# Performance work log

Hardware: AMD Instinct MI355X
Metric: run time of the kernel (lower is better)

The kernel has to match this reference:

```python
import jax, jax.numpy as jnp
import numpy as np

HEAD_SIZE = 12
INNER_DIM = 64
BIG_NEG = 1e12


def _sinusoidal(seq_len, dim):
    # interleaved [sin, cos, sin, cos, ...] like SinusoidalPositionEmbedding('zero')
    pos = jnp.arange(seq_len, dtype=jnp.float32)
    inv = jnp.power(10000.0, -2.0 * jnp.arange(dim // 2, dtype=jnp.float32) / dim)
    ang = pos[:, None] * inv[None, :]                       # (L, dim/2)
    return jnp.stack([jnp.sin(ang), jnp.cos(ang)], axis=-1).reshape(seq_len, dim)


def _rope_rotate(x, cos_pos, sin_pos):
    # x: (B, L, H, D); rotate-half per interleaved RoPE
    x2 = jnp.stack([-x[..., 1::2], x[..., ::2]], axis=-1).reshape(x.shape)
    return x * cos_pos + x2 * sin_pos


def setup_inputs() -> dict:
    key = jax.random.key(0)
    k1, k2 = jax.random.split(key)
    B, L, HID = 16, 512, 768
    sequence_output = jax.random.normal(k1, (B, L, HID), dtype=jnp.float32)
    mask = jnp.ones((B, L), dtype=jnp.float32)
    W = jax.random.normal(k2, (HID, HEAD_SIZE * INNER_DIM * 2), dtype=jnp.float32) * 0.02
    b = jnp.zeros((HEAD_SIZE * INNER_DIM * 2,), dtype=jnp.float32)
    return {"sequence_output": sequence_output, "mask": mask, "W": W, "b": b}


def reference(sequence_output, mask, W, b):
    B, L, _ = sequence_output.shape
    H, D = HEAD_SIZE, INNER_DIM
    out = sequence_output @ W + b                           # (B, L, H*2D)
    out = out.reshape(B, L, H, 2 * D)
    qw, kw = out[..., :D], out[..., D:]                     # (B, L, H, D)
    pos = _sinusoidal(L, D)                                 # (L, D)
    cos_pos = jnp.repeat(pos[:, None, 1::2], 2, axis=-1)    # (L, 1, D)
    sin_pos = jnp.repeat(pos[:, None, ::2], 2, axis=-1)
    qw = _rope_rotate(qw, cos_pos, sin_pos)
    kw = _rope_rotate(kw, cos_pos, sin_pos)
    logits = jnp.einsum('bmhd,bnhd->bhmn', qw, kw)          # (B, H, L, L)
    pad = mask[:, None, None, :]                            # (B, 1, 1, L)
    logits = logits * pad - (1.0 - pad) * BIG_NEG
    tril = jnp.tril(jnp.ones((L, L), dtype=logits.dtype), -1)
    logits = logits - tril * BIG_NEG
    return logits / (D ** 0.5)
```

## Files before the change

### kernel.cpp

```cpp
#include <hip/hip_runtime.h>
#include <stdint.h>

typedef float f32x4 __attribute__((ext_vector_type(4)));
typedef unsigned long long u64;

#define HEADS 12
#define DDIM 64
#define LSEQ 512
#define HID 768
#define NOUT 1536
#define BIG_NEG 1000000000000.0f

__device__ __forceinline__ void gl_lds16(const void* g, void* l) {
    __builtin_amdgcn_global_load_lds(
        (const __attribute__((address_space(1))) void*)g,
        (__attribute__((address_space(3))) void*)l, 16, 0, 0);
}

__device__ __forceinline__ void ldsbar() {
    asm volatile("s_waitcnt lgkmcnt(0)" ::: "memory");
    __builtin_amdgcn_s_barrier();
}

__device__ __forceinline__ uint32_t pk4_fp8(float a, float b, float c, float d) {
    uint32_t v = __builtin_amdgcn_cvt_pk_fp8_f32(a, b, 0, false);
    v = __builtin_amdgcn_cvt_pk_fp8_f32(c, d, v, true);
    return v;
}

__global__ __launch_bounds__(256) void prep_k(
    const float* __restrict__ X, const float* __restrict__ W,
    uint8_t* __restrict__ Xq, uint8_t* __restrict__ Wtq,
    float* __restrict__ cosT, float* __restrict__ sinT) {

    int blk = blockIdx.x;
    if (blk < 3072) {
        size_t idx = ((size_t)blk * 256 + threadIdx.x) * 8;
        float4 f0 = *(const float4*)(X + idx);
        float4 f1 = *(const float4*)(X + idx + 4);
        uint2 p;
        p.x = pk4_fp8(f0.x, f0.y, f0.z, f0.w);
        p.y = pk4_fp8(f1.x, f1.y, f1.z, f1.w);
        *(uint2*)(Xq + idx) = p;
    } else if (blk < 4224) {
        __shared__ float Ls[32][33];
        int b2 = blk - 3072;
        int n0 = (b2 % 48) * 32, k0 = (b2 / 48) * 32;
        int tx = threadIdx.x & 31, ty = threadIdx.x >> 5;
#pragma unroll
        for (int rr = 0; rr < 4; ++rr) {
            int k = ty + rr * 8;
            Ls[k][tx] = W[(size_t)(k0 + k) * NOUT + n0 + tx];
        }
        __syncthreads();
        int n = threadIdx.x >> 3, c = threadIdx.x & 7;
        uint32_t w = pk4_fp8(Ls[4*c][n], Ls[4*c+1][n], Ls[4*c+2][n], Ls[4*c+3][n]);
        *(uint32_t*)(Wtq + (size_t)(n0 + n) * HID + k0 + c * 4) = w;
    } else {
        int idx = (blk - 4224) * 256 + threadIdx.x;
        int l = idx >> 6, d = idx & 63;
        int p = d >> 1;
        float inv = powf(10000.0f, (-2.0f * (float)p) / 64.0f);
        float ang = (float)l * inv;
        cosT[idx] = cosf(ang);
        sinT[idx] = sinf(ang);
    }
}

__global__ __launch_bounds__(256) void proj_rope_k(
    const uint8_t* __restrict__ Xq, const uint8_t* __restrict__ Wtq,
    const float* __restrict__ bias, const float* __restrict__ cosT,
    const float* __restrict__ sinT,
    uint8_t* __restrict__ qq, uint8_t* __restrict__ kq) {

    __shared__ __align__(16) uint8_t As[128 * 64];
    __shared__ __align__(16) uint8_t Bs[128 * 64];

    const int tid = threadIdx.x;
    const int m0 = blockIdx.x * 128, n0 = blockIdx.y * 128;
    const int lane = tid & 63, wid = tid >> 6;
    const int wm = wid >> 1, wn = wid & 1;
    const int lr = lane & 15, kg = lane >> 4;

    const int srow = tid >> 2, sc = tid & 3;

    f32x4 acc[4][4] = {};

    for (int k0 = 0; k0 < HID; k0 += 64) {
#pragma unroll
        for (int j = 0; j < 2; ++j) {
            int r = j * 64 + srow;
            int cs = sc ^ ((r >> 1) & 3);
            gl_lds16(Wtq + (size_t)(n0 + r) * HID + k0 + cs * 16,
                     Bs + j * 4096 + tid * 16);
            gl_lds16(Xq + (size_t)(m0 + r) * HID + k0 + cs * 16,
                     As + j * 4096 + tid * 16);
        }
        __syncthreads();
#pragma unroll
        for (int ks = 0; ks < 2; ++ks) {
            u64 af[4], xf[4];
#pragma unroll
            for (int ai = 0; ai < 4; ++ai) {
                int row = wn * 64 + ai * 16 + lr;
                int sl = (ks * 4 + kg) ^ (row & 6);
                af[ai] = *(const u64*)(Bs + row * 64 + sl * 8);
            }
#pragma unroll
            for (int bi = 0; bi < 4; ++bi) {
                int row = wm * 64 + bi * 16 + lr;
                int sl = (ks * 4 + kg) ^ (row & 6);
                xf[bi] = *(const u64*)(As + row * 64 + sl * 8);
            }
#pragma unroll
            for (int ai = 0; ai < 4; ++ai)
#pragma unroll
                for (int bi = 0; bi < 4; ++bi)
                    acc[ai][bi] = __builtin_amdgcn_mfma_f32_16x16x32_fp8_fp8(
                        (long long)af[ai], (long long)xf[bi], acc[ai][bi], 0, 0, 0);
        }
        __syncthreads();
    }

#pragma unroll
    for (int ai = 0; ai < 4; ++ai) {
        int nb = n0 + wn * 64 + ai * 16 + kg * 4;
        int h = nb >> 7, d2 = nb & 127;
        int d = d2 & 63;
        uint8_t* dst = (d2 >= 64) ? kq : qq;
        float4 b4 = *(const float4*)&bias[nb];
#pragma unroll
        for (int bi = 0; bi < 4; ++bi) {
            int m = m0 + wm * 64 + bi * 16 + lr;
            int bidx = m >> 9, lpos = m & 511;
            float4 c4 = *(const float4*)&cosT[lpos * 64 + d];
            float4 s4 = *(const float4*)&sinT[lpos * 64 + d];
            float v0 = acc[ai][bi][0] + b4.x;
            float v1 = acc[ai][bi][1] + b4.y;
            float v2 = acc[ai][bi][2] + b4.z;
            float v3 = acc[ai][bi][3] + b4.w;
            float o0 = v0 * c4.x - v1 * s4.x;
            float o1 = v1 * c4.y + v0 * s4.y;
            float o2 = v2 * c4.z - v3 * s4.z;
            float o3 = v3 * c4.w + v2 * s4.w;
            uint32_t pw = pk4_fp8(o0, o1, o2, o3);
            *(uint32_t*)(dst + (((size_t)bidx * HEADS + h) * LSEQ + lpos) * DDIM + d) = pw;
        }
    }
}

__global__ __launch_bounds__(256) void attn_k(
    const uint8_t* __restrict__ qq, const uint8_t* __restrict__ kq,
    const float* __restrict__ mask, float* __restrict__ out) {

    __shared__ __align__(16) uint8_t Qs[8192];
    __shared__ __align__(16) uint8_t Ks[8192];
    __shared__ __align__(16) float Es[32 * 132];
    __shared__ int wok[4];

    const int tid = threadIdx.x;
    const int bid = blockIdx.x;
    const int L = (bid & 7) * 96 + (bid >> 3);
    const int bh = L >> 2;
    const int mtile = L & 3;
    const int m0 = mtile * 128;
    const int lane = tid & 63, wid = tid >> 6;
    const int wm = wid >> 1, wn = wid & 1;
    const int lr = lane & 15, kg = lane >> 4;
    const int b = bh / HEADS;

    int myok = 1;
    for (int c0 = tid; c0 < m0; c0 += 256)
        myok &= (mask[b * LSEQ + c0] == 1.0f) ? 1 : 0;
    unsigned long long bal = __ballot(myok);
    if (lane == 0) wok[wid] = (bal == ~0ull) ? 1 : 0;
    ldsbar();
    const int nstart = (wok[0] & wok[1] & wok[2] & wok[3]) ? mtile : 0;

    const uint8_t* qbase = qq + ((size_t)bh * LSEQ + m0) * DDIM;
    const uint8_t* kbase = kq + (size_t)bh * LSEQ * DDIM;

    const int srow = tid >> 2, sc = tid & 3;
#pragma unroll
    for (int j = 0; j < 2; ++j) {
        int r = j * 64 + srow;
        int cs = sc ^ ((r >> 1) & 3);
        gl_lds16(qbase + (size_t)r * DDIM + cs * 16, Qs + j * 4096 + tid * 16);
        gl_lds16(kbase + (size_t)(nstart * 128 + r) * DDIM + cs * 16,
                 Ks + j * 4096 + tid * 16);
    }
    __syncthreads();

    const int colb = (tid & 31) * 4;
    const int rrow = tid >> 5;
    float* obase = out + (size_t)bh * LSEQ * LSEQ;

    for (int nt = nstart; nt < 4; ++nt) {
        f32x4 acc[4][4] = {};
#pragma unroll
        for (int ks = 0; ks < 2; ++ks) {
            u64 af[4], qf[4];
#pragma unroll
            for (int ai = 0; ai < 4; ++ai) {
                int row = wn * 64 + ai * 16 + lr;
                int sl = (ks * 4 + kg) ^ (row & 6);
                af[ai] = *(const u64*)(Ks + row * 64 + sl * 8);
            }
#pragma unroll
            for (int bi = 0; bi < 4; ++bi) {
                int row = wm * 64 + bi * 16 + lr;
                int sl = (ks * 4 + kg) ^ (row & 6);
                qf[bi] = *(const u64*)(Qs + row * 64 + sl * 8);
            }
#pragma unroll
            for (int ai = 0; ai < 4; ++ai)
#pragma unroll
                for (int bi = 0; bi < 4; ++bi)
                    acc[ai][bi] = __builtin_amdgcn_mfma_f32_16x16x32_fp8_fp8(
                        (long long)af[ai], (long long)qf[bi], acc[ai][bi], 0, 0, 0);
        }
        ldsbar();

        const int n0 = nt * 128;
        const float4 p4 = *(const float4*)&mask[b * LSEQ + n0 + colb];

        if (nt < 3) {
#pragma unroll
            for (int j = 0; j < 2; ++j) {
                int r = j * 64 + srow;
                int cs = sc ^ ((r >> 1) & 3);
                gl_lds16(kbase + (size_t)((nt + 1) * 128 + r) * DDIM + cs * 16,
                         Ks + j * 4096 + tid * 16);
            }
        }

#pragma unroll
        for (int p = 0; p < 4; ++p) {
            ldsbar();
            if (wm == (p >> 1)) {
                const int bi0 = (p & 1) * 2;
#pragma unroll
                for (int bb = 0; bb < 2; ++bb) {
                    int bi = bi0 + bb;
                    int row = bb * 16 + lr;
#pragma unroll
                    for (int ai = 0; ai < 4; ++ai) {
                        int n = wn * 64 + ai * 16 + kg * 4;
                        *(f32x4*)&Es[row * 132 + n] = acc[ai][bi];
                    }
                }
            }
            ldsbar();
#pragma unroll
            for (int j = 0; j < 4; ++j) {
                int rloc = rrow + j * 8;
                int m = m0 + p * 32 + rloc;
                f32x4 v = *(f32x4*)&Es[rloc * 132 + colb];
                int n = n0 + colb;
                f32x4 o;
                o[0] = (v[0] * p4.x - (1.0f - p4.x) * BIG_NEG
                        - ((m > n + 0) ? BIG_NEG : 0.0f)) * 0.125f;
                o[1] = (v[1] * p4.y - (1.0f - p4.y) * BIG_NEG
                        - ((m > n + 1) ? BIG_NEG : 0.0f)) * 0.125f;
                o[2] = (v[2] * p4.z - (1.0f - p4.z) * BIG_NEG
                        - ((m > n + 2) ? BIG_NEG : 0.0f)) * 0.125f;
                o[3] = (v[3] * p4.w - (1.0f - p4.w) * BIG_NEG
                        - ((m > n + 3) ? BIG_NEG : 0.0f)) * 0.125f;
                __builtin_nontemporal_store(o, (f32x4*)&obase[(size_t)m * LSEQ + n]);
            }
        }

        if (nt < 3) {
            asm volatile("s_waitcnt vmcnt(16) lgkmcnt(0)" ::: "memory");
            __builtin_amdgcn_s_barrier();
        }
    }

    const float CONSTV = (-BIG_NEG) * 0.125f;
    f32x4 cv = {CONSTV, CONSTV, CONSTV, CONSTV};
    for (int nt2 = 0; nt2 < nstart; ++nt2) {
        int n = nt2 * 128 + colb;
#pragma unroll
        for (int p = 0; p < 4; ++p)
#pragma unroll
            for (int j = 0; j < 4; ++j) {
                int m = m0 + p * 32 + rrow + j * 8;
                __builtin_nontemporal_store(cv, (f32x4*)&obase[(size_t)m * LSEQ + n]);
            }
    }
}

extern "C" void kernel_launch(void* const* d_in, const int* in_sizes, int n_in,
                              void* d_out, int out_size, void* d_ws, size_t ws_size,
                              hipStream_t stream) {
    const float* X    = (const float*)d_in[0];
    const float* mask = (const float*)d_in[1];
    const float* W    = (const float*)d_in[2];
    const float* bias = (const float*)d_in[3];
    float* out = (float*)d_out;

    char* ws = (char*)d_ws;
    float*   cosT = (float*)ws;
    float*   sinT = (float*)(ws + 131072);
    uint8_t* Wtq  = (uint8_t*)(ws + 262144);
    uint8_t* Xq   = (uint8_t*)(ws + 1441792);
    uint8_t* qq   = (uint8_t*)(ws + 7733248);
    uint8_t* kq   = (uint8_t*)(ws + 14024704);

    prep_k<<<4352, 256, 0, stream>>>(X, W, Xq, Wtq, cosT, sinT);
    proj_rope_k<<<dim3(64, 12), 256, 0, stream>>>(Xq, Wtq, bias, cosT, sinT, qq, kq);
    attn_k<<<768, 256, 0, stream>>>(qq, kq, mask, out);
}
```

Baseline: 83.54 us.

## Use 32x32 fp8 MFMA with Q in registers and direct scalar output stores

Rewrites the attention-logit kernel so each wave owns 32 query rows held in registers and runs 32x32x16 fp8 MFMAs against K tiles in LDS. The LDS staging buffer and its barrier-heavy transpose epilogue are dropped in favor of storing accumulators straight to global memory as scalar nontemporal stores. It also adds a fast path for an all-ones mask that skips the padding arithmetic. The cost removed is LDS round trips and barriers in the epilogue, at the price of 4-byte stores that coalesce only 32 floats per row instead of 16-byte vector stores.

```diff
diff --git a/kernel.cpp b/kernel.cpp
--- a/kernel.cpp
+++ b/kernel.cpp
@@ -2,6 +2,7 @@
 #include <stdint.h>
 
 typedef float f32x4 __attribute__((ext_vector_type(4)));
+typedef float f32x16 __attribute__((ext_vector_type(16)));
 typedef unsigned long long u64;
 
 #define HEADS 12
@@ -10,6 +11,7 @@
 #define HID 768
 #define NOUT 1536
 #define BIG_NEG 1000000000000.0f
+#define BIGS 125000000000.0f
 
 __device__ __forceinline__ void gl_lds16(const void* g, void* l) {
     __builtin_amdgcn_global_load_lds(
@@ -153,10 +155,9 @@
     const uint8_t* __restrict__ qq, const uint8_t* __restrict__ kq,
     const float* __restrict__ mask, float* __restrict__ out) {
 
-    __shared__ __align__(16) uint8_t Qs[8192];
     __shared__ __align__(16) uint8_t Ks[8192];
-    __shared__ __align__(16) float Es[32 * 132];
     __shared__ int wok[4];
+    __shared__ int wall[4];
 
     const int tid = threadIdx.x;
     const int bid = blockIdx.x;
@@ -165,19 +166,23 @@
     const int mtile = L & 3;
     const int m0 = mtile * 128;
     const int lane = tid & 63, wid = tid >> 6;
-    const int wm = wid >> 1, wn = wid & 1;
-    const int lr = lane & 15, kg = lane >> 4;
+    const int li = lane & 31, hi = lane >> 5;
     const int b = bh / HEADS;
 
-    int myok = 1;
-    for (int c0 = tid; c0 < m0; c0 += 256)
-        myok &= (mask[b * LSEQ + c0] == 1.0f) ? 1 : 0;
-    unsigned long long bal = __ballot(myok);
-    if (lane == 0) wok[wid] = (bal == ~0ull) ? 1 : 0;
+    int myok = 1, myall = 1;
+    for (int c0 = tid; c0 < LSEQ; c0 += 256) {
+        int one = (mask[b * LSEQ + c0] == 1.0f) ? 1 : 0;
+        myall &= one;
+        if (c0 < m0) myok &= one;
+    }
+    unsigned long long balok = __ballot(myok);
+    unsigned long long balall = __ballot(myall);
+    if (lane == 0) { wok[wid] = (balok == ~0ull); wall[wid] = (balall == ~0ull); }
     ldsbar();
     const int nstart = (wok[0] & wok[1] & wok[2] & wok[3]) ? mtile : 0;
-
-    const uint8_t* qbase = qq + ((size_t)bh * LSEQ + m0) * DDIM;
+    const int allones = wall[0] & wall[1] & wall[2] & wall[3];
+
+    const uint8_t* qbase = qq + ((size_t)bh * LSEQ + m0 + wid * 32) * DDIM;
     const uint8_t* kbase = kq + (size_t)bh * LSEQ * DDIM;
 
     const int srow = tid >> 2, sc = tid & 3;
@@ -185,44 +190,34 @@
     for (int j = 0; j < 2; ++j) {
         int r = j * 64 + srow;
         int cs = sc ^ ((r >> 1) & 3);
-        gl_lds16(qbase + (size_t)r * DDIM + cs * 16, Qs + j * 4096 + tid * 16);
         gl_lds16(kbase + (size_t)(nstart * 128 + r) * DDIM + cs * 16,
                  Ks + j * 4096 + tid * 16);
     }
+
+    u64 qf[4];
+#pragma unroll
+    for (int ks = 0; ks < 4; ++ks)
+        qf[ks] = *(const u64*)(qbase + (size_t)li * DDIM + ks * 16 + hi * 8);
+
     __syncthreads();
 
-    const int colb = (tid & 31) * 4;
-    const int rrow = tid >> 5;
     float* obase = out + (size_t)bh * LSEQ * LSEQ;
+    float* lanebase = obase + (size_t)(m0 + wid * 32 + hi * 4) * LSEQ + li;
 
     for (int nt = nstart; nt < 4; ++nt) {
-        f32x4 acc[4][4] = {};
-#pragma unroll
-        for (int ks = 0; ks < 2; ++ks) {
-            u64 af[4], qf[4];
-#pragma unroll
-            for (int ai = 0; ai < 4; ++ai) {
-                int row = wn * 64 + ai * 16 + lr;
-                int sl = (ks * 4 + kg) ^ (row & 6);
-                af[ai] = *(const u64*)(Ks + row * 64 + sl * 8);
-            }
-#pragma unroll
-            for (int bi = 0; bi < 4; ++bi) {
-                int row = wm * 64 + bi * 16 + lr;
-                int sl = (ks * 4 + kg) ^ (row & 6);
-                qf[bi] = *(const u64*)(Qs + row * 64 + sl * 8);
-            }
-#pragma unroll
-            for (int ai = 0; ai < 4; ++ai)
-#pragma unroll
-                for (int bi = 0; bi < 4; ++bi)
-                    acc[ai][bi] = __builtin_amdgcn_mfma_f32_16x16x32_fp8_fp8(
-                        (long long)af[ai], (long long)qf[bi], acc[ai][bi], 0, 0, 0);
+        f32x16 acc[4] = {};
+#pragma unroll
+        for (int ks = 0; ks < 4; ++ks) {
+#pragma unroll
+            for (int ni = 0; ni < 4; ++ni) {
+                int row = ni * 32 + li;
+                int sl = (ks * 2 + hi) ^ (row & 6);
+                u64 kf = *(const u64*)(Ks + row * 64 + sl * 8);
+                acc[ni] = __builtin_amdgcn_mfma_f32_32x32x16_fp8_fp8(
+                    (long long)qf[ks], (long long)kf, acc[ni], 0, 0, 0);
+            }
         }
         ldsbar();
-
-        const int n0 = nt * 128;
-        const float4 p4 = *(const float4*)&mask[b * LSEQ + n0 + colb];
 
         if (nt < 3) {
 #pragma unroll
@@ -234,39 +229,49 @@
             }
         }
 
-#pragma unroll
-        for (int p = 0; p < 4; ++p) {
-            ldsbar();
-            if (wm == (p >> 1)) {
-                const int bi0 = (p & 1) * 2;
-#pragma unroll
-                for (int bb = 0; bb < 2; ++bb) {
-                    int bi = bi0 + bb;
-                    int row = bb * 16 + lr;
-#pragma unroll
-                    for (int ai = 0; ai < 4; ++ai) {
-                        int n = wn * 64 + ai * 16 + kg * 4;
-                        *(f32x4*)&Es[row * 132 + n] = acc[ai][bi];
+        const int n0t = nt * 128;
+        if (allones) {
+            if (nt != mtile) {
+#pragma unroll
+                for (int ni = 0; ni < 4; ++ni)
+#pragma unroll
+                    for (int rg = 0; rg < 16; ++rg) {
+                        int roff = (rg & 3) + 8 * (rg >> 2);
+                        float o = acc[ni][rg] * 0.125f;
+                        __builtin_nontemporal_store(o,
+                            lanebase + (size_t)roff * LSEQ + n0t + ni * 32);
+                    }
+            } else {
+                const int mbase = m0 + wid * 32 + hi * 4;
+#pragma unroll
+                for (int ni = 0; ni < 4; ++ni) {
+                    int nl = n0t + ni * 32 + li;
+#pragma unroll
+                    for (int rg = 0; rg < 16; ++rg) {
+                        int roff = (rg & 3) + 8 * (rg >> 2);
+                        float o = acc[ni][rg] * 0.125f
+                                  - (((mbase + roff) > nl) ? BIGS : 0.0f);
+                        __builtin_nontemporal_store(o,
+                            lanebase + (size_t)roff * LSEQ + n0t + ni * 32);
                     }
                 }
             }
-            ldsbar();
-#pragma unroll
-            for (int j = 0; j < 4; ++j) {
-                int rloc = rrow + j * 8;
-                int m = m0 + p * 32 + rloc;
-                f32x4 v = *(f32x4*)&Es[rloc * 132 + colb];
-                int n = n0 + colb;
-                f32x4 o;
-                o[0] = (v[0] * p4.x - (1.0f - p4.x) * BIG_NEG
-                        - ((m > n + 0) ? BIG_NEG : 0.0f)) * 0.125f;
-                o[1] = (v[1] * p4.y - (1.0f - p4.y) * BIG_NEG
-                        - ((m > n + 1) ? BIG_NEG : 0.0f)) * 0.125f;
-                o[2] = (v[2] * p4.z - (1.0f - p4.z) * BIG_NEG
-                        - ((m > n + 2) ? BIG_NEG : 0.0f)) * 0.125f;
-                o[3] = (v[3] * p4.w - (1.0f - p4.w) * BIG_NEG
-                        - ((m > n + 3) ? BIG_NEG : 0.0f)) * 0.125f;
-                __builtin_nontemporal_store(o, (f32x4*)&obase[(size_t)m * LSEQ + n]);
+        } else {
+            const int mbase = m0 + wid * 32 + hi * 4;
+#pragma unroll
+            for (int ni = 0; ni < 4; ++ni) {
+                int nl = n0t + ni * 32 + li;
+                float pad = mask[b * LSEQ + nl];
+                float c1 = pad * 0.125f;
+                float c2 = (pad - 1.0f) * BIGS;
+#pragma unroll
+                for (int rg = 0; rg < 16; ++rg) {
+                    int roff = (rg & 3) + 8 * (rg >> 2);
+                    float o = acc[ni][rg] * c1 + c2
+                              - (((mbase + roff) > nl) ? BIGS : 0.0f);
+                    __builtin_nontemporal_store(o,
+                        lanebase + (size_t)roff * LSEQ + n0t + ni * 32);
+                }
             }
         }
 
@@ -276,17 +281,11 @@
         }
     }
 
-    const float CONSTV = (-BIG_NEG) * 0.125f;
-    f32x4 cv = {CONSTV, CONSTV, CONSTV, CONSTV};
-    for (int nt2 = 0; nt2 < nstart; ++nt2) {
-        int n = nt2 * 128 + colb;
-#pragma unroll
-        for (int p = 0; p < 4; ++p)
-#pragma unroll
-            for (int j = 0; j < 4; ++j) {
-                int m = m0 + p * 32 + rrow + j * 8;
-                __builtin_nontemporal_store(cv, (f32x4*)&obase[(size_t)m * LSEQ + n]);
-            }
+    if (nstart > 0) {
+        float* fb = obase + (size_t)(m0 + wid * 32) * LSEQ + lane;
+        for (int mr = 0; mr < 32; ++mr)
+            for (int nn = 0; nn < nstart * 128; nn += 64)
+                __builtin_nontemporal_store(-BIGS, fb + (size_t)mr * LSEQ + nn);
     }
 }
 
```

Measured after the change: 87.78 us. +5.1%, slower.

## Use per-wave LDS staging for epilogue transpose to drop block barriers

Applied to the files above, without the earlier changes.

Replaces the shared 32x132 epilogue staging buffer, which needed two block-wide barriers per 32-row pass with only half the waves writing, with a private 16x68 buffer per wave. Each wave now transposes its own accumulator tiles through LDS and writes 64-float-wide rows of output directly. This removes the block barriers in the store phase and lets all waves store at once. The trade-off is shorter contiguous store runs (256 bytes per row instead of 512) and no explicit intra-wave fence between the LDS write and read.

```diff
diff --git a/kernel.cpp b/kernel.cpp
--- a/kernel.cpp
+++ b/kernel.cpp
@@ -155,7 +155,7 @@
 
     __shared__ __align__(16) uint8_t Qs[8192];
     __shared__ __align__(16) uint8_t Ks[8192];
-    __shared__ __align__(16) float Es[32 * 132];
+    __shared__ __align__(16) float Esw[4][16 * 68];
     __shared__ int wok[4];
 
     const int tid = threadIdx.x;
@@ -191,8 +191,6 @@
     }
     __syncthreads();
 
-    const int colb = (tid & 31) * 4;
-    const int rrow = tid >> 5;
     float* obase = out + (size_t)bh * LSEQ * LSEQ;
 
     for (int nt = nstart; nt < 4; ++nt) {
@@ -221,8 +219,7 @@
         }
         ldsbar();
 
-        const int n0 = nt * 128;
-        const float4 p4 = *(const float4*)&mask[b * LSEQ + n0 + colb];
+        const int n0t = nt * 128;
 
         if (nt < 3) {
 #pragma unroll
@@ -234,29 +231,20 @@
             }
         }
 
-#pragma unroll
-        for (int p = 0; p < 4; ++p) {
-            ldsbar();
-            if (wm == (p >> 1)) {
-                const int bi0 = (p & 1) * 2;
-#pragma unroll
-                for (int bb = 0; bb < 2; ++bb) {
-                    int bi = bi0 + bb;
-                    int row = bb * 16 + lr;
-#pragma unroll
-                    for (int ai = 0; ai < 4; ++ai) {
-                        int n = wn * 64 + ai * 16 + kg * 4;
-                        *(f32x4*)&Es[row * 132 + n] = acc[ai][bi];
-                    }
-                }
-            }
-            ldsbar();
+        const float4 p4 = *(const float4*)&mask[b * LSEQ + n0t + wn * 64 + lr * 4];
+        float* wavebase = obase + (size_t)(m0 + wm * 64) * LSEQ + n0t + wn * 64;
+
+#pragma unroll
+        for (int bi = 0; bi < 4; ++bi) {
+#pragma unroll
+            for (int ai = 0; ai < 4; ++ai)
+                *(f32x4*)&Esw[wid][lr * 68 + ai * 16 + kg * 4] = acc[ai][bi];
 #pragma unroll
             for (int j = 0; j < 4; ++j) {
-                int rloc = rrow + j * 8;
-                int m = m0 + p * 32 + rloc;
-                f32x4 v = *(f32x4*)&Es[rloc * 132 + colb];
-                int n = n0 + colb;
+                int rl = j * 4 + kg;
+                f32x4 v = *(f32x4*)&Esw[wid][rl * 68 + lr * 4];
+                int m = m0 + wm * 64 + bi * 16 + rl;
+                int n = n0t + wn * 64 + lr * 4;
                 f32x4 o;
                 o[0] = (v[0] * p4.x - (1.0f - p4.x) * BIG_NEG
                         - ((m > n + 0) ? BIG_NEG : 0.0f)) * 0.125f;
@@ -266,7 +254,7 @@
                         - ((m > n + 2) ? BIG_NEG : 0.0f)) * 0.125f;
                 o[3] = (v[3] * p4.w - (1.0f - p4.w) * BIG_NEG
                         - ((m > n + 3) ? BIG_NEG : 0.0f)) * 0.125f;
-                __builtin_nontemporal_store(o, (f32x4*)&obase[(size_t)m * LSEQ + n]);
+                __builtin_nontemporal_store(o, (f32x4*)&wavebase[(size_t)(bi * 16 + rl) * LSEQ + lr * 4]);
             }
         }
 
@@ -278,6 +266,8 @@
 
     const float CONSTV = (-BIG_NEG) * 0.125f;
     f32x4 cv = {CONSTV, CONSTV, CONSTV, CONSTV};
+    const int colb = (tid & 31) * 4;
+    const int rrow = tid >> 5;
     for (int nt2 = 0; nt2 < nstart; ++nt2) {
         int n = nt2 * 128 + colb;
 #pragma unroll
```

Result: slower. 85.71 us (+2.6%).

## Double-buffer K tiles, keep Q fragments in registers, fast path for all-ones mask

Applied to the files above, without the earlier changes.

K tiles are now double-buffered in LDS, so the next tile's global-to-LDS load is issued before the current tile's MFMAs and no longer waits behind the epilogue. Q fragments are loaded once straight from global into registers instead of being staged through LDS. A block-wide check for an all-ones mask enables a simpler epilogue that skips the mask loads and applies the causal penalty only on the diagonal tile. This adds LDS usage and hand-tuned vmcnt waits that must match the number of outstanding stores and loads.

```diff
diff --git a/kernel.cpp b/kernel.cpp
--- a/kernel.cpp
+++ b/kernel.cpp
@@ -10,6 +10,7 @@
 #define HID 768
 #define NOUT 1536
 #define BIG_NEG 1000000000000.0f
+#define BIGS 125000000000.0f
 
 __device__ __forceinline__ void gl_lds16(const void* g, void* l) {
     __builtin_amdgcn_global_load_lds(
@@ -153,10 +154,10 @@
     const uint8_t* __restrict__ qq, const uint8_t* __restrict__ kq,
     const float* __restrict__ mask, float* __restrict__ out) {
 
-    __shared__ __align__(16) uint8_t Qs[8192];
-    __shared__ __align__(16) uint8_t Ks[8192];
+    __shared__ __align__(16) uint8_t Ks[2][8192];
     __shared__ __align__(16) float Es[32 * 132];
     __shared__ int wok[4];
+    __shared__ int wall[4];
 
     const int tid = threadIdx.x;
     const int bid = blockIdx.x;
@@ -169,13 +170,18 @@
     const int lr = lane & 15, kg = lane >> 4;
     const int b = bh / HEADS;
 
-    int myok = 1;
-    for (int c0 = tid; c0 < m0; c0 += 256)
-        myok &= (mask[b * LSEQ + c0] == 1.0f) ? 1 : 0;
-    unsigned long long bal = __ballot(myok);
-    if (lane == 0) wok[wid] = (bal == ~0ull) ? 1 : 0;
+    int myok = 1, myall = 1;
+    for (int c0 = tid; c0 < LSEQ; c0 += 256) {
+        int one = (mask[b * LSEQ + c0] == 1.0f) ? 1 : 0;
+        myall &= one;
+        if (c0 < m0) myok &= one;
+    }
+    unsigned long long balok = __ballot(myok);
+    unsigned long long balall = __ballot(myall);
+    if (lane == 0) { wok[wid] = (balok == ~0ull); wall[wid] = (balall == ~0ull); }
     ldsbar();
     const int nstart = (wok[0] & wok[1] & wok[2] & wok[3]) ? mtile : 0;
+    const int allones = wall[0] & wall[1] & wall[2] & wall[3];
 
     const uint8_t* qbase = qq + ((size_t)bh * LSEQ + m0) * DDIM;
     const uint8_t* kbase = kq + (size_t)bh * LSEQ * DDIM;
@@ -185,10 +191,18 @@
     for (int j = 0; j < 2; ++j) {
         int r = j * 64 + srow;
         int cs = sc ^ ((r >> 1) & 3);
-        gl_lds16(qbase + (size_t)r * DDIM + cs * 16, Qs + j * 4096 + tid * 16);
         gl_lds16(kbase + (size_t)(nstart * 128 + r) * DDIM + cs * 16,
-                 Ks + j * 4096 + tid * 16);
-    }
+                 Ks[0] + j * 4096 + tid * 16);
+    }
+
+    u64 qf[2][4];
+#pragma unroll
+    for (int ks = 0; ks < 2; ++ks)
+#pragma unroll
+        for (int bi = 0; bi < 4; ++bi)
+            qf[ks][bi] = *(const u64*)(qbase + (size_t)(wm * 64 + bi * 16 + lr) * DDIM
+                                       + (ks * 4 + kg) * 8);
+
     __syncthreads();
 
     const int colb = (tid & 31) * 4;
@@ -196,43 +210,42 @@
     float* obase = out + (size_t)bh * LSEQ * LSEQ;
 
     for (int nt = nstart; nt < 4; ++nt) {
-        f32x4 acc[4][4] = {};
-#pragma unroll
-        for (int ks = 0; ks < 2; ++ks) {
-            u64 af[4], qf[4];
-#pragma unroll
-            for (int ai = 0; ai < 4; ++ai) {
-                int row = wn * 64 + ai * 16 + lr;
-                int sl = (ks * 4 + kg) ^ (row & 6);
-                af[ai] = *(const u64*)(Ks + row * 64 + sl * 8);
-            }
-#pragma unroll
-            for (int bi = 0; bi < 4; ++bi) {
-                int row = wm * 64 + bi * 16 + lr;
-                int sl = (ks * 4 + kg) ^ (row & 6);
-                qf[bi] = *(const u64*)(Qs + row * 64 + sl * 8);
-            }
-#pragma unroll
-            for (int ai = 0; ai < 4; ++ai)
-#pragma unroll
-                for (int bi = 0; bi < 4; ++bi)
-                    acc[ai][bi] = __builtin_amdgcn_mfma_f32_16x16x32_fp8_fp8(
-                        (long long)af[ai], (long long)qf[bi], acc[ai][bi], 0, 0, 0);
-        }
-        ldsbar();
-
-        const int n0 = nt * 128;
-        const float4 p4 = *(const float4*)&mask[b * LSEQ + n0 + colb];
-
+        const int cur = (nt - nstart) & 1;
+        if (nt > nstart) {
+            asm volatile("s_waitcnt vmcnt(17) lgkmcnt(0)" ::: "memory");
+            __builtin_amdgcn_s_barrier();
+        }
         if (nt < 3) {
 #pragma unroll
             for (int j = 0; j < 2; ++j) {
                 int r = j * 64 + srow;
                 int cs = sc ^ ((r >> 1) & 3);
                 gl_lds16(kbase + (size_t)((nt + 1) * 128 + r) * DDIM + cs * 16,
-                         Ks + j * 4096 + tid * 16);
-            }
-        }
+                         Ks[cur ^ 1] + j * 4096 + tid * 16);
+            }
+        }
+
+        f32x4 acc[4][4] = {};
+#pragma unroll
+        for (int ks = 0; ks < 2; ++ks) {
+            u64 af[4];
+#pragma unroll
+            for (int ai = 0; ai < 4; ++ai) {
+                int row = wn * 64 + ai * 16 + lr;
+                int sl = (ks * 4 + kg) ^ (row & 6);
+                af[ai] = *(const u64*)(Ks[cur] + row * 64 + sl * 8);
+            }
+#pragma unroll
+            for (int ai = 0; ai < 4; ++ai)
+#pragma unroll
+                for (int bi = 0; bi < 4; ++bi)
+                    acc[ai][bi] = __builtin_amdgcn_mfma_f32_16x16x32_fp8_fp8(
+                        (long long)af[ai], (long long)qf[ks][bi], acc[ai][bi], 0, 0, 0);
+        }
+
+        const int n0t = nt * 128;
+        float4 p4;
+        if (!allones) p4 = *(const float4*)&mask[b * LSEQ + n0t + colb];
 
 #pragma unroll
         for (int p = 0; p < 4; ++p) {
@@ -256,28 +269,33 @@
                 int rloc = rrow + j * 8;
                 int m = m0 + p * 32 + rloc;
                 f32x4 v = *(f32x4*)&Es[rloc * 132 + colb];
-                int n = n0 + colb;
+                int n = n0t + colb;
                 f32x4 o;
-                o[0] = (v[0] * p4.x - (1.0f - p4.x) * BIG_NEG
-                        - ((m > n + 0) ? BIG_NEG : 0.0f)) * 0.125f;
-                o[1] = (v[1] * p4.y - (1.0f - p4.y) * BIG_NEG
-                        - ((m > n + 1) ? BIG_NEG : 0.0f)) * 0.125f;
-                o[2] = (v[2] * p4.z - (1.0f - p4.z) * BIG_NEG
-                        - ((m > n + 2) ? BIG_NEG : 0.0f)) * 0.125f;
-                o[3] = (v[3] * p4.w - (1.0f - p4.w) * BIG_NEG
-                        - ((m > n + 3) ? BIG_NEG : 0.0f)) * 0.125f;
+                if (allones) {
+                    if (nt != mtile) {
+#pragma unroll
+                        for (int i = 0; i < 4; ++i) o[i] = v[i] * 0.125f;
+                    } else {
+#pragma unroll
+                        for (int i = 0; i < 4; ++i)
+                            o[i] = v[i] * 0.125f - ((m > n + i) ? BIGS : 0.0f);
+                    }
+                } else {
+                    o[0] = (v[0] * p4.x - (1.0f - p4.x) * BIG_NEG
+                            - ((m > n + 0) ? BIG_NEG : 0.0f)) * 0.125f;
+                    o[1] = (v[1] * p4.y - (1.0f - p4.y) * BIG_NEG
+                            - ((m > n + 1) ? BIG_NEG : 0.0f)) * 0.125f;
+                    o[2] = (v[2] * p4.z - (1.0f - p4.z) * BIG_NEG
+                            - ((m > n + 2) ? BIG_NEG : 0.0f)) * 0.125f;
+                    o[3] = (v[3] * p4.w - (1.0f - p4.w) * BIG_NEG
+                            - ((m > n + 3) ? BIG_NEG : 0.0f)) * 0.125f;
+                }
                 __builtin_nontemporal_store(o, (f32x4*)&obase[(size_t)m * LSEQ + n]);
             }
         }
-
-        if (nt < 3) {
-            asm volatile("s_waitcnt vmcnt(16) lgkmcnt(0)" ::: "memory");
-            __builtin_amdgcn_s_barrier();
-        }
-    }
-
-    const float CONSTV = (-BIG_NEG) * 0.125f;
-    f32x4 cv = {CONSTV, CONSTV, CONSTV, CONSTV};
+    }
+
+    f32x4 cv = {-BIGS, -BIGS, -BIGS, -BIGS};
     for (int nt2 = 0; nt2 < nstart; ++nt2) {
         int n = nt2 * 128 + colb;
 #pragma unroll
```

After: 86.81 us. +3.9%, slower.
